# Performance work log

Measured on AMD Instinct MI355X. Metric: run time of the kernel, lower is better.

Reference implementation:

```python
import jax, jax.numpy as jnp
import numpy as np

N_USERS = 100_000
N_ITEMS = 50_000
N = N_USERS + N_ITEMS
N_LAYERS = 3
ALPHA = 0.8
D = 64
IMG_D = 4096
TXT_D = 384
N_INTER = 2_000_000  # user-item interactions; symmetric nnz = 2*N_INTER


def setup_inputs() -> dict:
    # --- build symmetric-normalized bipartite adjacency (D^-1/2 A D^-1/2) in numpy ---
    rng = np.random.default_rng(0)
    u = rng.integers(0, N_USERS, N_INTER).astype(np.int32)
    i = (rng.integers(0, N_ITEMS, N_INTER) + N_USERS).astype(np.int32)
    rows = np.concatenate([u, i])
    cols = np.concatenate([i, u])
    deg = np.bincount(rows, minlength=N).astype(np.float32)
    d_inv = np.where(deg > 0, deg ** -0.5, 0.0).astype(np.float32)
    vals = d_inv[rows] * d_inv[cols]

    key = jax.random.key(0)
    ks = jax.random.split(key, 8)
    xav_img = float(np.sqrt(6.0 / (IMG_D + D)))
    xav_txt = float(np.sqrt(6.0 / (TXT_D + D)))
    return {
        "image_feats": jax.random.normal(ks[0], (N_ITEMS, IMG_D), jnp.float32),
        "text_feats": jax.random.normal(ks[1], (N_ITEMS, TXT_D), jnp.float32),
        "image_pref": jax.random.normal(ks[2], (N_USERS, D), jnp.float32),
        "text_pref": jax.random.normal(ks[3], (N_USERS, D), jnp.float32),
        "W_img": jax.random.uniform(ks[4], (IMG_D, D), jnp.float32, -xav_img, xav_img),
        "b_img": jnp.zeros((D,), jnp.float32),
        "W_txt": jax.random.uniform(ks[5], (TXT_D, D), jnp.float32, -xav_txt, xav_txt),
        "b_txt": jnp.zeros((D,), jnp.float32),
        "adj_vals": jnp.asarray(vals),
        "adj_rows": jnp.asarray(rows),
        "adj_cols": jnp.asarray(cols),
    }


def _spmm(rows, cols, vals, x):
    # sparse COO @ dense: out[r] += vals[e] * x[cols[e]]
    return jax.ops.segment_sum(vals[:, None] * x[cols], rows, num_segments=N)


def _l2norm(x):
    # F.normalize(x, dim=1): row-wise L2 with eps clamp
    return x / jnp.clip(jnp.linalg.norm(x, axis=1, keepdims=True), 1e-12)


def reference(image_feats, text_feats, image_pref, text_pref,
              W_img, b_img, W_txt, b_txt, adj_vals, adj_rows, adj_cols):
    img = _l2norm(image_feats @ W_img + b_img)   # [n_items, D]
    txt = _l2norm(text_feats @ W_txt + b_txt)    # [n_items, D]
    ego_i = jnp.concatenate([image_pref, img], axis=0)  # [N, D]
    ego_t = jnp.concatenate([text_pref, txt], axis=0)   # [N, D]
    for _ in range(N_LAYERS):
        ego_i = _spmm(adj_rows, adj_cols, adj_vals, ego_i) + ALPHA * ego_i
        ego_t = _spmm(adj_rows, adj_cols, adj_vals, ego_t) + ALPHA * ego_t
    user_preference = jnp.concatenate([ego_i[:N_USERS], ego_t[:N_USERS]], axis=1)  # [n_users, 2D]
    items = jnp.concatenate([ego_i[N_USERS:], ego_t[N_USERS:]], axis=1)            # [n_items, 2D]
    return user_preference, items
```

## Files before the change

kernel.cpp:

```cpp
#include <hip/hip_runtime.h>
#include <hip/hip_bf16.h>

#define N_USERS 100000
#define N_ITEMS 50000
#define N_TOTAL 150000
#define NNZ     4000000
#define ALPHA_F 0.8f
#define ELL_CAP 128

#define G_SCAT 1024
#define G_COPY 128
#define G_PRE  (G_SCAT + G_COPY)
#define G_GEMM 3125
#define NC_IMG 64
#define NC_ALL 70

typedef __attribute__((ext_vector_type(8))) short bf16x8;
typedef __attribute__((ext_vector_type(4))) float f32x4;

static __device__ __forceinline__ short f2bf(float f) {
    unsigned u = __builtin_bit_cast(unsigned, f);
    unsigned r = (u + 0x7fff + ((u >> 16) & 1)) >> 16;
    return (short)r;
}
static __device__ __forceinline__ unsigned pack_bf2(float a, float b) {
    return (unsigned)(unsigned short)f2bf(a) | ((unsigned)(unsigned short)f2bf(b) << 16);
}
static __device__ __forceinline__ float bf_lo(unsigned u) { return __uint_as_float(u << 16); }
static __device__ __forceinline__ float bf_hi(unsigned u) { return __uint_as_float(u & 0xFFFF0000u); }

static __device__ __forceinline__ void gload_lds16(const void* src, void* dst) {
    __builtin_amdgcn_global_load_lds(
        (const __attribute__((address_space(1))) unsigned*)src,
        (__attribute__((address_space(3))) unsigned*)dst, 16, 0, 0);
}


__global__ __launch_bounds__(256) void prep_kernel(const float* __restrict__ Wimg,
                                                   const float* __restrict__ Wtxt,
                                                   int* __restrict__ cnt,
                                                   char* __restrict__ WtiT,
                                                   char* __restrict__ WttT) {
    const int T0 = N_TOTAL;
    const int T1 = T0 + 4096 * 64;
    const int T2 = T1 + 384 * 64;
    int i = blockIdx.x * 256 + threadIdx.x;
    int stride = gridDim.x * 256;
    for (; i < T2; i += stride) {
        if (i < T0) {
            cnt[i] = 0;
        } else if (i < T1) {
            int idx = i - T0; int k = idx >> 6, n = idx & 63;
            int c = k >> 6, kk = k & 63;
            *(short*)(WtiT + c * 8192 + n * 128 + ((kk * 2) ^ ((n & 7) << 4)))
                = f2bf(Wimg[(size_t)k * 64 + n]);
        } else {
            int idx = i - T1; int k = idx >> 6, n = idx & 63;
            int c = k >> 6, kk = k & 63;
            *(short*)(WttT + c * 8192 + n * 128 + ((kk * 2) ^ ((n & 7) << 4)))
                = f2bf(Wtxt[(size_t)k * 64 + n]);
        }
    }
}


__global__ __launch_bounds__(256, 6) void mega_kernel(
        const float* __restrict__ Aimg, const float* __restrict__ Atxt,
        const char* __restrict__ WtiT, const char* __restrict__ WttT,
        const float* __restrict__ bimg, const float* __restrict__ btxt,
        unsigned* __restrict__ egob,
        const int* __restrict__ rows, const int* __restrict__ cols,
        const float* __restrict__ vals, int* __restrict__ cnt, int2* __restrict__ ell,
        const float* __restrict__ img_pref, const float* __restrict__ txt_pref) {
    __shared__ __align__(16) char abuf[2][4096];
    __shared__ __align__(16) char bbuf[2][8192];
    int b = blockIdx.x;
    int t = threadIdx.x;
    int wave = t >> 6, lane = t & 63;

    if (b < G_SCAT) {
        int i = b * 256 + t;
        int stride = G_SCAT * 256;
        for (; i < NNZ; i += stride) {
            int r = rows[i];
            int p = atomicAdd(&cnt[r], 1);
            if (p < ELL_CAP)
                ell[(size_t)r * ELL_CAP + p] = make_int2(cols[i], __float_as_int(vals[i]));
        }
        return;
    }
    if (b < G_PRE) {
        int idx = (b - G_SCAT) * 256 + t;
        int stride = G_COPY * 256;
        for (; idx < N_USERS * 16; idx += stride) {
            int row = idx >> 4, w4 = (idx & 15) << 2;
            float4 iv = *reinterpret_cast<const float4*>(&img_pref[(size_t)row * 64 + w4]);
            float4 tv = *reinterpret_cast<const float4*>(&txt_pref[(size_t)row * 64 + w4]);
            uint4 m;
            m.x = pack_bf2(iv.x, tv.x); m.y = pack_bf2(iv.y, tv.y);
            m.z = pack_bf2(iv.z, tv.z); m.w = pack_bf2(iv.w, tv.w);
            *reinterpret_cast<uint4*>(&egob[(size_t)row * 64 + w4]) = m;
        }
        return;
    }

    const int blk = b - G_PRE;
    const int row0 = blk * 16;
    const int col = lane & 15, kb = lane >> 4;

    auto stage = [&](int ci, int bi) {
        const float* A; size_t rowbytes; const char* BT; int cc;
        if (ci < NC_IMG) { A = Aimg; rowbytes = 16384; BT = WtiT; cc = ci; }
        else             { A = Atxt; rowbytes = 1536;  BT = WttT; cc = ci - NC_IMG; }
        {
            int r = wave * 4 + (lane >> 4);
            int so = ((lane & 15) * 16) ^ ((r & 7) << 4);
            const char* src = (const char*)A + (size_t)(row0 + r) * rowbytes + cc * 256 + so;
            char* dst = abuf[bi] + wave * 1024 + lane * 16;
            gload_lds16(src, dst);
        }
        #pragma unroll
        for (int q = 0; q < 2; ++q) {
            int off = (q * 4 + wave) * 1024 + lane * 16;
            gload_lds16(BT + (size_t)cc * 8192 + off, bbuf[bi] + off);
        }
    };

    auto comp = [&](int bi, f32x4& acc) {
        const int r = col;
        const int aswz = (r & 7) << 4;
        const char* ab = abuf[bi] + r * 256;
        const int n = 16 * wave + col;
        const char* bb = bbuf[bi] + n * 128;
        const int bswz = (n & 7) << 4;
        #pragma unroll
        for (int ks = 0; ks < 2; ++ks) {
            int la = ks * 128 + kb * 32;
            float4 a0 = *(const float4*)(ab + (la ^ aswz));
            float4 a1 = *(const float4*)(ab + ((la + 16) ^ aswz));
            bf16x8 af;
            af[0]=f2bf(a0.x); af[1]=f2bf(a0.y); af[2]=f2bf(a0.z); af[3]=f2bf(a0.w);
            af[4]=f2bf(a1.x); af[5]=f2bf(a1.y); af[6]=f2bf(a1.z); af[7]=f2bf(a1.w);
            bf16x8 bf = *(const bf16x8*)(bb + ((ks * 64 + kb * 16) ^ bswz));
            acc = __builtin_amdgcn_mfma_f32_16x16x32_bf16(af, bf, acc, 0, 0, 0);
        }
    };

    f32x4 ai = {0.f,0.f,0.f,0.f}, at4 = {0.f,0.f,0.f,0.f};

    stage(0, 0);
    for (int ci = 0; ci < NC_ALL; ++ci) {
        int bi = ci & 1;
        if (ci + 1 < NC_ALL) {
            stage(ci + 1, bi ^ 1);
            asm volatile("s_waitcnt vmcnt(3)" ::: "memory");
        } else {
            asm volatile("s_waitcnt vmcnt(0)" ::: "memory");
        }
        __builtin_amdgcn_s_barrier();
        __builtin_amdgcn_sched_barrier(0);
        if (ci < NC_IMG) comp(bi, ai);
        else             comp(bi, at4);
        __builtin_amdgcn_sched_barrier(0);
        __builtin_amdgcn_s_barrier();
    }

    float bv_i = bimg[16 * wave + col];
    float bv_t = btxt[16 * wave + col];
    float ssi[4], sst[4];
    #pragma unroll
    for (int i = 0; i < 4; ++i) {
        ai[i] += bv_i; at4[i] += bv_t;
        ssi[i] = ai[i] * ai[i];
        sst[i] = at4[i] * at4[i];
    }
    #pragma unroll
    for (int off = 1; off < 16; off <<= 1) {
        #pragma unroll
        for (int i = 0; i < 4; ++i) {
            ssi[i] += __shfl_xor(ssi[i], off, 64);
            sst[i] += __shfl_xor(sst[i], off, 64);
        }
    }
    float* S = (float*)abuf;
    __syncthreads();
    if (col == 0) {
        #pragma unroll
        for (int i = 0; i < 4; ++i) {
            S[wave * 16 + kb * 4 + i]      = ssi[i];
            S[64 + wave * 16 + kb * 4 + i] = sst[i];
        }
    }
    __syncthreads();
    unsigned* egob_items = egob + (size_t)N_USERS * 64;
    #pragma unroll
    for (int i = 0; i < 4; ++i) {
        int r = kb * 4 + i;
        float ti = S[r] + S[16 + r] + S[32 + r] + S[48 + r];
        float tt = S[64 + r] + S[80 + r] + S[96 + r] + S[112 + r];
        float rni = 1.0f / fmaxf(sqrtf(ti), 1e-12f);
        float rnt = 1.0f / fmaxf(sqrtf(tt), 1e-12f);
        egob_items[(size_t)(row0 + r) * 64 + 16 * wave + col] =
            pack_bf2(ai[i] * rni, at4[i] * rnt);
    }
}


__global__ __launch_bounds__(256) void spmm_sort_kernel(
        const int* __restrict__ cnt, int2* __restrict__ ell,
        const unsigned* __restrict__ xb, unsigned* __restrict__ outb) {
    __shared__ __align__(16) int2 srt[4][ELL_CAP];
    int wid = threadIdx.x >> 6, lane = threadIdx.x & 63;
    int row = blockIdx.x * 4 + wid;
    bool valid = row < N_TOTAL;
    int deg = 0;
    int2* base = nullptr;
    int2 e0 = make_int2(0x7FFFFFFF, 0), e1 = e0;
    if (valid) {
        deg = min(cnt[row], ELL_CAP);
        base = ell + (size_t)row * ELL_CAP;
        if (lane < deg)      e0 = base[lane];
        if (lane + 64 < deg) e1 = base[lane + 64];
    }
    #pragma unroll
    for (int k = 2; k <= 128; k <<= 1) {
        #pragma unroll
        for (int j = 64; j >= 1; j >>= 1) {
            if (j >= k) continue;
            if (j == 64) {
                if (e0.x > e1.x) { int2 tmp = e0; e0 = e1; e1 = tmp; }
            } else {
                int2 p0, p1;
                p0.x = __shfl_xor(e0.x, j, 64); p0.y = __shfl_xor(e0.y, j, 64);
                p1.x = __shfl_xor(e1.x, j, 64); p1.y = __shfl_xor(e1.y, j, 64);
                bool up0 = ((lane & k) == 0);
                bool up1 = (((lane + 64) & k) == 0);
                bool lo0 = ((lane & j) == 0);
                bool keepmin0 = (up0 == lo0);
                bool keepmin1 = (up1 == lo0);
                if (keepmin0 ? (e0.x > p0.x) : (e0.x < p0.x)) e0 = p0;
                if (keepmin1 ? (e1.x > p1.x) : (e1.x < p1.x)) e1 = p1;
            }
        }
    }
    if (valid) {
        if (lane < deg)      base[lane]      = e0;
        if (lane + 64 < deg) base[lane + 64] = e1;
    }
    srt[wid][lane] = e0;
    srt[wid][lane + 64] = e1;
    __syncthreads();
    if (!valid) return;
    unsigned sw = xb[(size_t)row * 64 + lane];
    float2 acc;
    acc.x = ALPHA_F * bf_lo(sw);
    acc.y = ALPHA_F * bf_hi(sw);
    const int2* s = srt[wid];
    int i = 0;
    for (; i + 8 <= deg; i += 8) {
        int4 p0 = *reinterpret_cast<const int4*>(s + i);
        int4 p1 = *reinterpret_cast<const int4*>(s + i + 2);
        int4 p2 = *reinterpret_cast<const int4*>(s + i + 4);
        int4 p3 = *reinterpret_cast<const int4*>(s + i + 6);
        unsigned g0 = xb[(size_t)p0.x * 64 + lane];
        unsigned g1 = xb[(size_t)p0.z * 64 + lane];
        unsigned g2 = xb[(size_t)p1.x * 64 + lane];
        unsigned g3 = xb[(size_t)p1.z * 64 + lane];
        unsigned g4 = xb[(size_t)p2.x * 64 + lane];
        unsigned g5 = xb[(size_t)p2.z * 64 + lane];
        unsigned g6 = xb[(size_t)p3.x * 64 + lane];
        unsigned g7 = xb[(size_t)p3.z * 64 + lane];
        float v0 = __int_as_float(p0.y), v1 = __int_as_float(p0.w);
        float v2 = __int_as_float(p1.y), v3 = __int_as_float(p1.w);
        float v4 = __int_as_float(p2.y), v5 = __int_as_float(p2.w);
        float v6 = __int_as_float(p3.y), v7 = __int_as_float(p3.w);
        acc.x = fmaf(v0, bf_lo(g0), acc.x); acc.y = fmaf(v0, bf_hi(g0), acc.y);
        acc.x = fmaf(v1, bf_lo(g1), acc.x); acc.y = fmaf(v1, bf_hi(g1), acc.y);
        acc.x = fmaf(v2, bf_lo(g2), acc.x); acc.y = fmaf(v2, bf_hi(g2), acc.y);
        acc.x = fmaf(v3, bf_lo(g3), acc.x); acc.y = fmaf(v3, bf_hi(g3), acc.y);
        acc.x = fmaf(v4, bf_lo(g4), acc.x); acc.y = fmaf(v4, bf_hi(g4), acc.y);
        acc.x = fmaf(v5, bf_lo(g5), acc.x); acc.y = fmaf(v5, bf_hi(g5), acc.y);
        acc.x = fmaf(v6, bf_lo(g6), acc.x); acc.y = fmaf(v6, bf_hi(g6), acc.y);
        acc.x = fmaf(v7, bf_lo(g7), acc.x); acc.y = fmaf(v7, bf_hi(g7), acc.y);
    }
    for (; i < deg; ++i) {
        int2 c = s[i];
        float v = __int_as_float(c.y);
        unsigned g = xb[(size_t)c.x * 64 + lane];
        acc.x = fmaf(v, bf_lo(g), acc.x);
        acc.y = fmaf(v, bf_hi(g), acc.y);
    }
    outb[(size_t)row * 64 + lane] = pack_bf2(acc.x, acc.y);
}


__global__ __launch_bounds__(256) void spmm2_kernel(
        const int* __restrict__ cnt, const int2* __restrict__ ell,
        const unsigned* __restrict__ xb,
        float* __restrict__ out32, unsigned* __restrict__ outb) {
    int wid = threadIdx.x >> 6, lane = threadIdx.x & 63;
    int rowA = blockIdx.x * 8 + wid * 2;
    int rowB = rowA + 1;
    int degA = min(cnt[rowA], ELL_CAP);
    int degB = min(cnt[rowB], ELL_CAP);
    const int2* baseA = ell + (size_t)rowA * ELL_CAP;
    const int2* baseB = ell + (size_t)rowB * ELL_CAP;
    unsigned swA = xb[(size_t)rowA * 64 + lane];
    unsigned swB = xb[(size_t)rowB * 64 + lane];
    float2 accA, accB;
    accA.x = ALPHA_F * bf_lo(swA); accA.y = ALPHA_F * bf_hi(swA);
    accB.x = ALPHA_F * bf_lo(swB); accB.y = ALPHA_F * bf_hi(swB);
    int dmax = max(degA, degB);
    for (int i = 0; i < dmax; i += 8) {
        int4 pa0 = *reinterpret_cast<const int4*>(baseA + i);
        int4 pa1 = *reinterpret_cast<const int4*>(baseA + i + 2);
        int4 pa2 = *reinterpret_cast<const int4*>(baseA + i + 4);
        int4 pa3 = *reinterpret_cast<const int4*>(baseA + i + 6);
        int4 pb0 = *reinterpret_cast<const int4*>(baseB + i);
        int4 pb1 = *reinterpret_cast<const int4*>(baseB + i + 2);
        int4 pb2 = *reinterpret_cast<const int4*>(baseB + i + 4);
        int4 pb3 = *reinterpret_cast<const int4*>(baseB + i + 6);
        int ca0 = (i+0<degA)?pa0.x:0; float va0 = (i+0<degA)?__int_as_float(pa0.y):0.f;
        int ca1 = (i+1<degA)?pa0.z:0; float va1 = (i+1<degA)?__int_as_float(pa0.w):0.f;
        int ca2 = (i+2<degA)?pa1.x:0; float va2 = (i+2<degA)?__int_as_float(pa1.y):0.f;
        int ca3 = (i+3<degA)?pa1.z:0; float va3 = (i+3<degA)?__int_as_float(pa1.w):0.f;
        int ca4 = (i+4<degA)?pa2.x:0; float va4 = (i+4<degA)?__int_as_float(pa2.y):0.f;
        int ca5 = (i+5<degA)?pa2.z:0; float va5 = (i+5<degA)?__int_as_float(pa2.w):0.f;
        int ca6 = (i+6<degA)?pa3.x:0; float va6 = (i+6<degA)?__int_as_float(pa3.y):0.f;
        int ca7 = (i+7<degA)?pa3.z:0; float va7 = (i+7<degA)?__int_as_float(pa3.w):0.f;
        int cb0 = (i+0<degB)?pb0.x:0; float vb0 = (i+0<degB)?__int_as_float(pb0.y):0.f;
        int cb1 = (i+1<degB)?pb0.z:0; float vb1 = (i+1<degB)?__int_as_float(pb0.w):0.f;
        int cb2 = (i+2<degB)?pb1.x:0; float vb2 = (i+2<degB)?__int_as_float(pb1.y):0.f;
        int cb3 = (i+3<degB)?pb1.z:0; float vb3 = (i+3<degB)?__int_as_float(pb1.w):0.f;
        int cb4 = (i+4<degB)?pb2.x:0; float vb4 = (i+4<degB)?__int_as_float(pb2.y):0.f;
        int cb5 = (i+5<degB)?pb2.z:0; float vb5 = (i+5<degB)?__int_as_float(pb2.w):0.f;
        int cb6 = (i+6<degB)?pb3.x:0; float vb6 = (i+6<degB)?__int_as_float(pb3.y):0.f;
        int cb7 = (i+7<degB)?pb3.z:0; float vb7 = (i+7<degB)?__int_as_float(pb3.w):0.f;
        unsigned ga0 = xb[(size_t)ca0 * 64 + lane];
        unsigned ga1 = xb[(size_t)ca1 * 64 + lane];
        unsigned ga2 = xb[(size_t)ca2 * 64 + lane];
        unsigned ga3 = xb[(size_t)ca3 * 64 + lane];
        unsigned ga4 = xb[(size_t)ca4 * 64 + lane];
        unsigned ga5 = xb[(size_t)ca5 * 64 + lane];
        unsigned ga6 = xb[(size_t)ca6 * 64 + lane];
        unsigned ga7 = xb[(size_t)ca7 * 64 + lane];
        unsigned gb0 = xb[(size_t)cb0 * 64 + lane];
        unsigned gb1 = xb[(size_t)cb1 * 64 + lane];
        unsigned gb2 = xb[(size_t)cb2 * 64 + lane];
        unsigned gb3 = xb[(size_t)cb3 * 64 + lane];
        unsigned gb4 = xb[(size_t)cb4 * 64 + lane];
        unsigned gb5 = xb[(size_t)cb5 * 64 + lane];
        unsigned gb6 = xb[(size_t)cb6 * 64 + lane];
        unsigned gb7 = xb[(size_t)cb7 * 64 + lane];
        accA.x = fmaf(va0, bf_lo(ga0), accA.x); accA.y = fmaf(va0, bf_hi(ga0), accA.y);
        accA.x = fmaf(va1, bf_lo(ga1), accA.x); accA.y = fmaf(va1, bf_hi(ga1), accA.y);
        accA.x = fmaf(va2, bf_lo(ga2), accA.x); accA.y = fmaf(va2, bf_hi(ga2), accA.y);
        accA.x = fmaf(va3, bf_lo(ga3), accA.x); accA.y = fmaf(va3, bf_hi(ga3), accA.y);
        accA.x = fmaf(va4, bf_lo(ga4), accA.x); accA.y = fmaf(va4, bf_hi(ga4), accA.y);
        accA.x = fmaf(va5, bf_lo(ga5), accA.x); accA.y = fmaf(va5, bf_hi(ga5), accA.y);
        accA.x = fmaf(va6, bf_lo(ga6), accA.x); accA.y = fmaf(va6, bf_hi(ga6), accA.y);
        accA.x = fmaf(va7, bf_lo(ga7), accA.x); accA.y = fmaf(va7, bf_hi(ga7), accA.y);
        accB.x = fmaf(vb0, bf_lo(gb0), accB.x); accB.y = fmaf(vb0, bf_hi(gb0), accB.y);
        accB.x = fmaf(vb1, bf_lo(gb1), accB.x); accB.y = fmaf(vb1, bf_hi(gb1), accB.y);
        accB.x = fmaf(vb2, bf_lo(gb2), accB.x); accB.y = fmaf(vb2, bf_hi(gb2), accB.y);
        accB.x = fmaf(vb3, bf_lo(gb3), accB.x); accB.y = fmaf(vb3, bf_hi(gb3), accB.y);
        accB.x = fmaf(vb4, bf_lo(gb4), accB.x); accB.y = fmaf(vb4, bf_hi(gb4), accB.y);
        accB.x = fmaf(vb5, bf_lo(gb5), accB.x); accB.y = fmaf(vb5, bf_hi(gb5), accB.y);
        accB.x = fmaf(vb6, bf_lo(gb6), accB.x); accB.y = fmaf(vb6, bf_hi(gb6), accB.y);
        accB.x = fmaf(vb7, bf_lo(gb7), accB.x); accB.y = fmaf(vb7, bf_hi(gb7), accB.y);
    }
    if (out32) {
        out32[(size_t)rowA * 128 + lane] = accA.x;
        out32[(size_t)rowA * 128 + 64 + lane] = accA.y;
        out32[(size_t)rowB * 128 + lane] = accB.x;
        out32[(size_t)rowB * 128 + 64 + lane] = accB.y;
    }
    if (outb) {
        outb[(size_t)rowA * 64 + lane] = pack_bf2(accA.x, accA.y);
        outb[(size_t)rowB * 64 + lane] = pack_bf2(accB.x, accB.y);
    }
}


extern "C" void kernel_launch(void* const* d_in, const int* in_sizes, int n_in,
                              void* d_out, int out_size, void* d_ws, size_t ws_size,
                              hipStream_t stream) {
    const float* image_feats = (const float*)d_in[0];
    const float* text_feats  = (const float*)d_in[1];
    const float* image_pref  = (const float*)d_in[2];
    const float* text_pref   = (const float*)d_in[3];
    const float* W_img       = (const float*)d_in[4];
    const float* b_img       = (const float*)d_in[5];
    const float* W_txt       = (const float*)d_in[6];
    const float* b_txt       = (const float*)d_in[7];
    const float* adj_vals    = (const float*)d_in[8];
    const int*   adj_rows    = (const int*)d_in[9];
    const int*   adj_cols    = (const int*)d_in[10];

    float* out = (float*)d_out;

    char* ws = (char*)d_ws;
    size_t off = 0;
    auto alloc = [&](size_t bytes) { char* p = ws + off; off += (bytes + 255) & ~size_t(255); return p; };
    int*      cnt   = (int*)     alloc(N_TOTAL * sizeof(int));
    int2*     ell   = (int2*)    alloc((size_t)N_TOTAL * ELL_CAP * sizeof(int2));
    unsigned* m0    = (unsigned*)alloc((size_t)N_TOTAL * 64 * sizeof(unsigned));
    unsigned* m1    = (unsigned*)alloc((size_t)N_TOTAL * 64 * sizeof(unsigned));
    char*     WtiT  = (char*)    alloc((size_t)NC_IMG * 8192);
    char*     WttT  = (char*)    alloc((size_t)6 * 8192);
    (void)ws_size; (void)out_size; (void)n_in; (void)in_sizes;

    prep_kernel<<<512, 256, 0, stream>>>(W_img, W_txt, cnt, WtiT, WttT);

    mega_kernel<<<G_PRE + G_GEMM, 256, 0, stream>>>(
        image_feats, text_feats, WtiT, WttT, b_img, b_txt, m0,
        adj_rows, adj_cols, adj_vals, cnt, ell, image_pref, text_pref);

    const int ROW_GRID4 = (N_TOTAL + 3) / 4;
    const int ROW_GRID8 = N_TOTAL / 8;
    spmm_sort_kernel<<<ROW_GRID4, 256, 0, stream>>>(cnt, ell, m0, m1);
    spmm2_kernel<<<ROW_GRID8, 256, 0, stream>>>(cnt, ell, m1, nullptr, m0);
    spmm2_kernel<<<ROW_GRID8, 256, 0, stream>>>(cnt, ell, m0, out, nullptr);
}
```

Baseline: 961.5 us.

## Split GEMM into bf16 tile-prepacking pass and separate MFMA GEMM kernel

Adds a pass that converts image and text features from fp32 to bf16 and writes them into swizzled, per-block tile-contiguous chunks, fused with the existing scatter and copy work. The GEMM then runs as its own kernel with 128-wide K chunks and loads A tiles directly, so the inner loop no longer converts fp32 to bf16. This spends an extra full read of the ~820MB fp32 features plus a ~410MB bf16 write and read-back, in exchange for contiguous loads and fewer conversions in the GEMM loop.

```diff
diff --git a/kernel.cpp b/kernel.cpp
--- a/kernel.cpp
+++ b/kernel.cpp
@@ -8,12 +8,13 @@
 #define ALPHA_F 0.8f
 #define ELL_CAP 128
 
-#define G_SCAT 1024
-#define G_COPY 128
-#define G_PRE  (G_SCAT + G_COPY)
+#define X_SCAT 1024
+#define X_COPY 128
+#define X_TIMG 1024
+#define X_TTXT 128
 #define G_GEMM 3125
-#define NC_IMG 64
-#define NC_ALL 70
+#define NC_IMG 32
+#define NC_ALL 35
 
 typedef __attribute__((ext_vector_type(8))) short bf16x8;
 typedef __attribute__((ext_vector_type(4))) float f32x4;
@@ -51,36 +52,32 @@
             cnt[i] = 0;
         } else if (i < T1) {
             int idx = i - T0; int k = idx >> 6, n = idx & 63;
-            int c = k >> 6, kk = k & 63;
-            *(short*)(WtiT + c * 8192 + n * 128 + ((kk * 2) ^ ((n & 7) << 4)))
+            int c = k >> 7, kk = k & 127;
+            *(short*)(WtiT + c * 16384 + n * 256 + ((kk * 2) ^ ((n & 7) << 4)))
                 = f2bf(Wimg[(size_t)k * 64 + n]);
         } else {
             int idx = i - T1; int k = idx >> 6, n = idx & 63;
-            int c = k >> 6, kk = k & 63;
-            *(short*)(WttT + c * 8192 + n * 128 + ((kk * 2) ^ ((n & 7) << 4)))
+            int c = k >> 7, kk = k & 127;
+            *(short*)(WttT + c * 16384 + n * 256 + ((kk * 2) ^ ((n & 7) << 4)))
                 = f2bf(Wtxt[(size_t)k * 64 + n]);
         }
     }
 }
 
 
-__global__ __launch_bounds__(256, 6) void mega_kernel(
+__global__ __launch_bounds__(256) void xpose_kernel(
         const float* __restrict__ Aimg, const float* __restrict__ Atxt,
-        const char* __restrict__ WtiT, const char* __restrict__ WttT,
-        const float* __restrict__ bimg, const float* __restrict__ btxt,
-        unsigned* __restrict__ egob,
+        char* __restrict__ At,
         const int* __restrict__ rows, const int* __restrict__ cols,
         const float* __restrict__ vals, int* __restrict__ cnt, int2* __restrict__ ell,
-        const float* __restrict__ img_pref, const float* __restrict__ txt_pref) {
-    __shared__ __align__(16) char abuf[2][4096];
-    __shared__ __align__(16) char bbuf[2][8192];
+        const float* __restrict__ img_pref, const float* __restrict__ txt_pref,
+        unsigned* __restrict__ egob) {
     int b = blockIdx.x;
     int t = threadIdx.x;
-    int wave = t >> 6, lane = t & 63;
-
-    if (b < G_SCAT) {
+
+    if (b < X_SCAT) {
         int i = b * 256 + t;
-        int stride = G_SCAT * 256;
+        int stride = X_SCAT * 256;
         for (; i < NNZ; i += stride) {
             int r = rows[i];
             int p = atomicAdd(&cnt[r], 1);
@@ -89,9 +86,9 @@
         }
         return;
     }
-    if (b < G_PRE) {
-        int idx = (b - G_SCAT) * 256 + t;
-        int stride = G_COPY * 256;
+    if (b < X_SCAT + X_COPY) {
+        int idx = (b - X_SCAT) * 256 + t;
+        int stride = X_COPY * 256;
         for (; idx < N_USERS * 16; idx += stride) {
             int row = idx >> 4, w4 = (idx & 15) << 2;
             float4 iv = *reinterpret_cast<const float4*>(&img_pref[(size_t)row * 64 + w4]);
@@ -103,26 +100,73 @@
         }
         return;
     }
-
-    const int blk = b - G_PRE;
+    if (b < X_SCAT + X_COPY + X_TIMG) {
+        const float4* A4 = reinterpret_cast<const float4*>(Aimg);
+        const size_t NF4 = (size_t)N_ITEMS * 1024;
+        const size_t S = (size_t)X_TIMG * 256;
+        size_t g = (size_t)(b - X_SCAT - X_COPY) * 256 + t;
+        auto wr = [&](size_t gi, float4 v) {
+            unsigned f = (unsigned)(gi * 4);
+            unsigned r = f >> 12, k = f & 4095;
+            unsigned bb = r >> 4, rr = r & 15, cc = k >> 7, kk = k & 127;
+            char* dst = At + ((size_t)bb * 35 + cc) * 4096 + rr * 256
+                        + ((kk * 2) ^ ((rr & 7) << 4));
+            uint2 u; u.x = pack_bf2(v.x, v.y); u.y = pack_bf2(v.z, v.w);
+            *reinterpret_cast<uint2*>(dst) = u;
+        };
+        for (; g + 3 * S < NF4; g += 4 * S) {
+            float4 v0 = A4[g], v1 = A4[g + S], v2 = A4[g + 2 * S], v3 = A4[g + 3 * S];
+            wr(g, v0); wr(g + S, v1); wr(g + 2 * S, v2); wr(g + 3 * S, v3);
+        }
+        for (; g < NF4; g += S) wr(g, A4[g]);
+        return;
+    }
+    {
+        const float4* A4 = reinterpret_cast<const float4*>(Atxt);
+        const size_t NF4 = (size_t)N_ITEMS * 96;
+        const size_t S = (size_t)X_TTXT * 256;
+        size_t g = (size_t)(b - X_SCAT - X_COPY - X_TIMG) * 256 + t;
+        auto wr = [&](size_t gi, float4 v) {
+            unsigned f = (unsigned)(gi * 4);
+            unsigned r = f / 384, k = f - r * 384;
+            unsigned bb = r >> 4, rr = r & 15, cc = 32 + (k >> 7), kk = k & 127;
+            char* dst = At + ((size_t)bb * 35 + cc) * 4096 + rr * 256
+                        + ((kk * 2) ^ ((rr & 7) << 4));
+            uint2 u; u.x = pack_bf2(v.x, v.y); u.y = pack_bf2(v.z, v.w);
+            *reinterpret_cast<uint2*>(dst) = u;
+        };
+        for (; g + 3 * S < NF4; g += 4 * S) {
+            float4 v0 = A4[g], v1 = A4[g + S], v2 = A4[g + 2 * S], v3 = A4[g + 3 * S];
+            wr(g, v0); wr(g + S, v1); wr(g + 2 * S, v2); wr(g + 3 * S, v3);
+        }
+        for (; g < NF4; g += S) wr(g, A4[g]);
+        return;
+    }
+}
+
+
+__global__ __launch_bounds__(256, 4) void gemm_kernel(
+        const char* __restrict__ At,
+        const char* __restrict__ WtiT, const char* __restrict__ WttT,
+        const float* __restrict__ bimg, const float* __restrict__ btxt,
+        unsigned* __restrict__ egob_items) {
+    __shared__ __align__(16) char abuf[2][4096];
+    __shared__ __align__(16) char bbuf[2][16384];
+    const int t = threadIdx.x;
+    const int wave = t >> 6, lane = t & 63;
+    const int col = lane & 15, kb = lane >> 4;
+    const int blk = blockIdx.x;
     const int row0 = blk * 16;
-    const int col = lane & 15, kb = lane >> 4;
 
     auto stage = [&](int ci, int bi) {
-        const float* A; size_t rowbytes; const char* BT; int cc;
-        if (ci < NC_IMG) { A = Aimg; rowbytes = 16384; BT = WtiT; cc = ci; }
-        else             { A = Atxt; rowbytes = 1536;  BT = WttT; cc = ci - NC_IMG; }
-        {
-            int r = wave * 4 + (lane >> 4);
-            int so = ((lane & 15) * 16) ^ ((r & 7) << 4);
-            const char* src = (const char*)A + (size_t)(row0 + r) * rowbytes + cc * 256 + so;
-            char* dst = abuf[bi] + wave * 1024 + lane * 16;
-            gload_lds16(src, dst);
-        }
+        gload_lds16(At + ((size_t)blk * 35 + ci) * 4096 + wave * 1024 + lane * 16,
+                    abuf[bi] + wave * 1024 + lane * 16);
+        const char* BT = (ci < NC_IMG) ? WtiT + (size_t)ci * 16384
+                                       : WttT + (size_t)(ci - NC_IMG) * 16384;
         #pragma unroll
-        for (int q = 0; q < 2; ++q) {
+        for (int q = 0; q < 4; ++q) {
             int off = (q * 4 + wave) * 1024 + lane * 16;
-            gload_lds16(BT + (size_t)cc * 8192 + off, bbuf[bi] + off);
+            gload_lds16(BT + off, bbuf[bi] + off);
         }
     };
 
@@ -131,17 +175,13 @@
         const int aswz = (r & 7) << 4;
         const char* ab = abuf[bi] + r * 256;
         const int n = 16 * wave + col;
-        const char* bb = bbuf[bi] + n * 128;
+        const char* bb = bbuf[bi] + n * 256;
         const int bswz = (n & 7) << 4;
         #pragma unroll
-        for (int ks = 0; ks < 2; ++ks) {
-            int la = ks * 128 + kb * 32;
-            float4 a0 = *(const float4*)(ab + (la ^ aswz));
-            float4 a1 = *(const float4*)(ab + ((la + 16) ^ aswz));
-            bf16x8 af;
-            af[0]=f2bf(a0.x); af[1]=f2bf(a0.y); af[2]=f2bf(a0.z); af[3]=f2bf(a0.w);
-            af[4]=f2bf(a1.x); af[5]=f2bf(a1.y); af[6]=f2bf(a1.z); af[7]=f2bf(a1.w);
-            bf16x8 bf = *(const bf16x8*)(bb + ((ks * 64 + kb * 16) ^ bswz));
+        for (int ks = 0; ks < 4; ++ks) {
+            int o = ks * 64 + kb * 16;
+            bf16x8 af = *(const bf16x8*)(ab + (o ^ aswz));
+            bf16x8 bf = *(const bf16x8*)(bb + (o ^ bswz));
             acc = __builtin_amdgcn_mfma_f32_16x16x32_bf16(af, bf, acc, 0, 0, 0);
         }
     };
@@ -153,7 +193,7 @@
         int bi = ci & 1;
         if (ci + 1 < NC_ALL) {
             stage(ci + 1, bi ^ 1);
-            asm volatile("s_waitcnt vmcnt(3)" ::: "memory");
+            asm volatile("s_waitcnt vmcnt(5)" ::: "memory");
         } else {
             asm volatile("s_waitcnt vmcnt(0)" ::: "memory");
         }
@@ -192,7 +232,6 @@
         }
     }
     __syncthreads();
-    unsigned* egob_items = egob + (size_t)N_USERS * 64;
     #pragma unroll
     for (int i = 0; i < 4; ++i) {
         int r = kb * 4 + i;
@@ -406,15 +445,19 @@
     int2*     ell   = (int2*)    alloc((size_t)N_TOTAL * ELL_CAP * sizeof(int2));
     unsigned* m0    = (unsigned*)alloc((size_t)N_TOTAL * 64 * sizeof(unsigned));
     unsigned* m1    = (unsigned*)alloc((size_t)N_TOTAL * 64 * sizeof(unsigned));
-    char*     WtiT  = (char*)    alloc((size_t)NC_IMG * 8192);
-    char*     WttT  = (char*)    alloc((size_t)6 * 8192);
+    char*     WtiT  = (char*)    alloc((size_t)NC_IMG * 16384);
+    char*     WttT  = (char*)    alloc((size_t)3 * 16384);
+    char*     At    = (char*)    alloc((size_t)G_GEMM * 35 * 4096);
     (void)ws_size; (void)out_size; (void)n_in; (void)in_sizes;
 
     prep_kernel<<<512, 256, 0, stream>>>(W_img, W_txt, cnt, WtiT, WttT);
 
-    mega_kernel<<<G_PRE + G_GEMM, 256, 0, stream>>>(
-        image_feats, text_feats, WtiT, WttT, b_img, b_txt, m0,
-        adj_rows, adj_cols, adj_vals, cnt, ell, image_pref, text_pref);
+    xpose_kernel<<<X_SCAT + X_COPY + X_TIMG + X_TTXT, 256, 0, stream>>>(
+        image_feats, text_feats, At, adj_rows, adj_cols, adj_vals, cnt, ell,
+        image_pref, text_pref, m0);
+
+    unsigned* m0_items = m0 + (size_t)N_USERS * 64;
+    gemm_kernel<<<G_GEMM, 256, 0, stream>>>(At, WtiT, WttT, b_img, b_txt, m0_items);
 
     const int ROW_GRID4 = (N_TOTAL + 3) / 4;
     const int ROW_GRID8 = N_TOTAL / 8;
```

New measurement: 1.192 ms. 1.24x slower.
